# Kernel tuning notes

Measured on AMD Instinct MI355X. Metric: run time of the kernel, lower is better.

## Reference

```python
import jax, jax.numpy as jnp
import numpy as np

D_MODEL = 768
NUM_HEADS = 8
HEAD_DIM = D_MODEL // NUM_HEADS


def setup_inputs() -> dict:
    key = jax.random.key(0)
    ks = jax.random.split(key, 5)
    B, N = 4, 2048
    scale = 1.0 / np.sqrt(D_MODEL)
    return {
        "x": jax.random.normal(ks[0], (B, N, D_MODEL), dtype=jnp.float32),
        "W_qkv": jax.random.normal(ks[1], (D_MODEL, 3 * D_MODEL), dtype=jnp.float32) * scale,
        "b_qkv": jax.random.normal(ks[2], (3 * D_MODEL,), dtype=jnp.float32) * 0.01,
        "W_out": jax.random.normal(ks[3], (D_MODEL, D_MODEL), dtype=jnp.float32) * scale,
        "b_out": jax.random.normal(ks[4], (D_MODEL,), dtype=jnp.float32) * 0.01,
    }


def reference(x, W_qkv, b_qkv, W_out, b_out):
    B, N, _ = x.shape
    H, Dh = NUM_HEADS, HEAD_DIM
    # fused QKV projection: [B,N,3*D] -> [3,B,H,N,Dh]
    qkv = (x @ W_qkv + b_qkv).reshape(B, N, 3, H, Dh).transpose(2, 0, 3, 1, 4)
    q, k, v = qkv[0], qkv[1], qkv[2]
    # full NxN attention, as in the original (no masking)
    scores = jnp.einsum("bhnd,bhmd->bhnm", q, k) / jnp.sqrt(jnp.float32(Dh)).astype(x.dtype)
    weights = jax.nn.softmax(scores, axis=-1)
    out = jnp.einsum("bhnm,bhmd->bhnd", weights, v)  # [B,H,N,Dh]
    out = out.transpose(0, 2, 1, 3).reshape(B, N, H * Dh)
    return out @ W_out + b_out
```

## Files before the change

kernel.cpp:

```cpp
#include <hip/hip_runtime.h>
#include <hip/hip_bf16.h>
#include <math.h>

#define BB      4
#define NN      2048
#define DM      768
#define NH      8
#define DHH     96
#define BH      (BB*NH)
#define MROWS   (BB*NN)
#define NC_QKV  (3*DM)

typedef short v8s  __attribute__((ext_vector_type(8)));
typedef float v16f __attribute__((ext_vector_type(16)));
typedef unsigned int u32;

#define SCQ 0.14724599350930152f

static __device__ __forceinline__ ushort f2bf(float f) {
    __hip_bfloat16 h = __float2bfloat16(f);
    return *reinterpret_cast<ushort*>(&h);
}

static __device__ __forceinline__ void gload_lds16(const ushort* g, ushort* l) {
    __builtin_amdgcn_global_load_lds(
        (const __attribute__((address_space(1))) void*)g,
        (__attribute__((address_space(3))) void*)l, 16, 0, 0);
}

static __device__ __forceinline__ v8s pack_frag(u32 a, u32 b, u32 c, u32 d) {
    union { u32 u[4]; v8s s; } x;
    x.u[0] = a; x.u[1] = b; x.u[2] = c; x.u[3] = d;
    return x.s;
}

__global__ __launch_bounds__(256)
void conv_bf16(const float* __restrict__ in, ushort* __restrict__ out, int n8)
{
    int i = blockIdx.x * 256 + threadIdx.x;
    if (i >= n8) return;
    const float4* p = reinterpret_cast<const float4*>(in) + (size_t)i * 2;
    float4 a = p[0], b = p[1];
    ushort r[8] = {f2bf(a.x), f2bf(a.y), f2bf(a.z), f2bf(a.w),
                   f2bf(b.x), f2bf(b.y), f2bf(b.z), f2bf(b.w)};
    *reinterpret_cast<v8s*>(out + (size_t)i * 8) = *reinterpret_cast<v8s*>(r);
}

__global__ __launch_bounds__(256)
void convT_bf16(const float* __restrict__ W, ushort* __restrict__ Wt, int K, int N)
{
    __shared__ ushort t[32][33];
    const int k0 = blockIdx.x * 32, n0 = blockIdx.y * 32;
    const int tx = threadIdx.x & 31, ty = threadIdx.x >> 5;
    #pragma unroll
    for (int r = ty; r < 32; r += 8)
        t[tx][r] = f2bf(W[(size_t)(k0 + r) * N + n0 + tx]);
    __syncthreads();
    #pragma unroll
    for (int r = ty; r < 32; r += 8)
        Wt[(size_t)(n0 + r) * K + k0 + tx] = t[r][tx];
}

template<int SCATTER>
__global__ __launch_bounds__(256)
void gemm_mfma(const ushort* __restrict__ A, const ushort* __restrict__ Bt,
               const float* __restrict__ bias, void* __restrict__ outp,
               int K, int Ncols)
{
    __shared__ ushort As[8192];
    __shared__ ushort Bs[8192];

    const int tid  = threadIdx.x;
    const int lane = tid & 63;
    const int wv   = tid >> 6;
    const int l31  = lane & 31;
    const int lhi  = lane >> 5;
    const int wr   = wv >> 1, wc = wv & 1;
    const int row0 = blockIdx.x * 128;
    const int col0 = blockIdx.y * 128;

    v16f acc[2][2];
    #pragma unroll
    for (int mi = 0; mi < 2; ++mi)
        #pragma unroll
        for (int nj = 0; nj < 2; ++nj)
            #pragma unroll
            for (int i = 0; i < 16; ++i) acc[mi][nj][i] = 0.0f;

    for (int k0 = 0; k0 < K; k0 += 64) {
        #pragma unroll
        for (int c = 0; c < 4; ++c) {
            const int idx = (c * 4 + wv) * 64 + lane;
            const int s = idx >> 7, r = idx & 127;
            gload_lds16(&A [(size_t)(row0 + r) * K + k0 + s * 8], &As[(size_t)(c * 4 + wv) * 512]);
            gload_lds16(&Bt[(size_t)(col0 + r) * K + k0 + s * 8], &Bs[(size_t)(c * 4 + wv) * 512]);
        }
        __syncthreads();

        #pragma unroll
        for (int s16 = 0; s16 < 4; ++s16) {
            const int ks = s16 * 2 + lhi;
            v8s a0 = *reinterpret_cast<const v8s*>(&As[(size_t)(ks * 128 + 64 * wr + l31) * 8]);
            v8s a1 = *reinterpret_cast<const v8s*>(&As[(size_t)(ks * 128 + 64 * wr + 32 + l31) * 8]);
            v8s b0 = *reinterpret_cast<const v8s*>(&Bs[(size_t)(ks * 128 + 64 * wc + l31) * 8]);
            v8s b1 = *reinterpret_cast<const v8s*>(&Bs[(size_t)(ks * 128 + 64 * wc + 32 + l31) * 8]);
            acc[0][0] = __builtin_amdgcn_mfma_f32_32x32x16_bf16(a0, b0, acc[0][0], 0, 0, 0);
            acc[0][1] = __builtin_amdgcn_mfma_f32_32x32x16_bf16(a0, b1, acc[0][1], 0, 0, 0);
            acc[1][0] = __builtin_amdgcn_mfma_f32_32x32x16_bf16(a1, b0, acc[1][0], 0, 0, 0);
            acc[1][1] = __builtin_amdgcn_mfma_f32_32x32x16_bf16(a1, b1, acc[1][1], 0, 0, 0);
        }
        __syncthreads();
    }

    #pragma unroll
    for (int nj = 0; nj < 2; ++nj) {
        const int c = col0 + 64 * wc + 32 * nj + l31;
        const float bv = bias[c];
        #pragma unroll
        for (int mi = 0; mi < 2; ++mi) {
            #pragma unroll
            for (int r = 0; r < 16; ++r) {
                const int m = row0 + 64 * wr + 32 * mi + (r & 3) + 8 * (r >> 2) + 4 * lhi;
                float v = acc[mi][nj][r] + bv;
                if (SCATTER) {
                    const int s   = c / DM;
                    const int rem = c - s * DM;
                    const int h   = rem / DHH;
                    const int d   = rem - h * DHH;
                    const int b   = m >> 11;
                    const int n   = m & (NN - 1);
                    if (s == 0) v *= SCQ;
                    ((ushort*)outp)[((size_t)(s * BH + b * NH + h) * NN + n) * DHH + d] = f2bf(v);
                } else {
                    ((float*)outp)[(size_t)m * Ncols + c] = v;
                }
            }
        }
    }
}

__global__ __launch_bounds__(256)
void attn_mfma(const ushort* __restrict__ qkv, ushort* __restrict__ attnout)
{
    __shared__ ushort Ks[2][6144];
    __shared__ ushort Vt[2][96][72];

    const int tid  = threadIdx.x;
    const int lane = tid & 63;
    const int wv   = tid >> 6;
    const int l31  = lane & 31;
    const int lhi  = lane >> 5;
    const int q0   = blockIdx.x * 128;
    const int bh   = blockIdx.y;
    const int b    = bh >> 3, h = bh & 7;

    const ushort* Qg = qkv + (size_t)bh * NN * DHH;
    const ushort* Kg = qkv + ((size_t)BH + bh) * NN * DHH;
    const ushort* Vg = qkv + ((size_t)2 * BH + bh) * NN * DHH;

    const int qr = q0 + wv * 32 + l31;
    v8s qf[6];
    #pragma unroll
    for (int kt = 0; kt < 6; ++kt)
        qf[kt] = *reinterpret_cast<const v8s*>(&Qg[(size_t)qr * DHH + kt * 16 + lhi * 8]);

    v16f o[3];
    #pragma unroll
    for (int dt = 0; dt < 3; ++dt)
        #pragma unroll
        for (int i = 0; i < 16; ++i) o[dt][i] = 0.0f;
    float dsum = 0.0f;

    {
        v8s kr[3], vr[3];
        #pragma unroll
        for (int i = 0; i < 3; ++i) {
            kr[i] = *reinterpret_cast<const v8s*>(&Kg[(size_t)lane * DHH + (wv * 3 + i) * 8]);
            vr[i] = *reinterpret_cast<const v8s*>(&Vg[(size_t)lane * DHH + (i * 4 + wv) * 8]);
        }
        #pragma unroll
        for (int i = 0; i < 3; ++i) {
            *reinterpret_cast<v8s*>(&Ks[0][(wv * 3 + i) * 512 + lane * 8]) = kr[i];
            #pragma unroll
            for (int j = 0; j < 8; ++j)
                Vt[0][(i * 4 + wv) * 8 + j][lane] = (ushort)vr[i][j];
        }
    }
    __syncthreads();

    for (int t = 0; t < 32; ++t) {
        const int cur = t & 1, nxt = cur ^ 1;
        const int kbase = (t + 1) * 64;

        v8s kr0, kr1, kr2, vr0, vr1, vr2;
        if (t < 31) {
            const ushort* krow = &Kg[(size_t)(kbase + lane) * DHH];
            const ushort* vrow = &Vg[(size_t)(kbase + lane) * DHH];
            kr0 = *reinterpret_cast<const v8s*>(&krow[(wv * 3 + 0) * 8]);
            kr1 = *reinterpret_cast<const v8s*>(&krow[(wv * 3 + 1) * 8]);
            kr2 = *reinterpret_cast<const v8s*>(&krow[(wv * 3 + 2) * 8]);
            vr0 = *reinterpret_cast<const v8s*>(&vrow[(0 * 4 + wv) * 8]);
            vr1 = *reinterpret_cast<const v8s*>(&vrow[(1 * 4 + wv) * 8]);
            vr2 = *reinterpret_cast<const v8s*>(&vrow[(2 * 4 + wv) * 8]);
        }

        v8s pfrag[4];
        #pragma unroll
        for (int ct = 0; ct < 2; ++ct) {
            v16f s;
            #pragma unroll
            for (int i = 0; i < 16; ++i) s[i] = 0.0f;
            #pragma unroll
            for (int kt = 0; kt < 6; ++kt) {
                v8s kf = *reinterpret_cast<const v8s*>(
                    &Ks[cur][((kt * 2 + lhi) * 64 + ct * 32 + l31) * 8]);
                s = __builtin_amdgcn_mfma_f32_32x32x16_bf16(kf, qf[kt], s, 0, 0, 0);
            }
            float e[16];
            #pragma unroll
            for (int r = 0; r < 16; ++r) {
                e[r] = exp2f(s[r]);
                dsum += e[r];
            }
            u32 w[8];
            #pragma unroll
            for (int i = 0; i < 8; ++i)
                w[i] = (u32)f2bf(e[2 * i]) | ((u32)f2bf(e[2 * i + 1]) << 16);
            const u32 t0 = __shfl_xor(lhi ? w[0] : w[2], 32, 64);
            const u32 t1 = __shfl_xor(lhi ? w[1] : w[3], 32, 64);
            const u32 t2 = __shfl_xor(lhi ? w[4] : w[6], 32, 64);
            const u32 t3 = __shfl_xor(lhi ? w[5] : w[7], 32, 64);
            pfrag[2 * ct + 0] = lhi ? pack_frag(t0, t1, w[2], w[3])
                                    : pack_frag(w[0], w[1], t0, t1);
            pfrag[2 * ct + 1] = lhi ? pack_frag(t2, t3, w[6], w[7])
                                    : pack_frag(w[4], w[5], t2, t3);
        }

        #pragma unroll
        for (int dt = 0; dt < 3; ++dt) {
            #pragma unroll
            for (int ks = 0; ks < 4; ++ks) {
                v8s va = *reinterpret_cast<const v8s*>(
                    &Vt[cur][dt * 32 + l31][ks * 16 + lhi * 8]);
                o[dt] = __builtin_amdgcn_mfma_f32_32x32x16_bf16(va, pfrag[ks], o[dt], 0, 0, 0);
            }
        }

        if (t < 31) {
            *reinterpret_cast<v8s*>(&Ks[nxt][(wv * 3 + 0) * 512 + lane * 8]) = kr0;
            *reinterpret_cast<v8s*>(&Ks[nxt][(wv * 3 + 1) * 512 + lane * 8]) = kr1;
            *reinterpret_cast<v8s*>(&Ks[nxt][(wv * 3 + 2) * 512 + lane * 8]) = kr2;
            #pragma unroll
            for (int j = 0; j < 8; ++j) Vt[nxt][(0 * 4 + wv) * 8 + j][lane] = (ushort)vr0[j];
            #pragma unroll
            for (int j = 0; j < 8; ++j) Vt[nxt][(1 * 4 + wv) * 8 + j][lane] = (ushort)vr1[j];
            #pragma unroll
            for (int j = 0; j < 8; ++j) Vt[nxt][(2 * 4 + wv) * 8 + j][lane] = (ushort)vr2[j];
        }
        __syncthreads();
    }

    dsum += __shfl_xor(dsum, 32, 64);
    const float inv = 1.0f / dsum;

    const int n = q0 + wv * 32 + l31;
    ushort* orow = attnout + ((size_t)(b * NN + n)) * DM + h * DHH;
    #pragma unroll
    for (int dt = 0; dt < 3; ++dt) {
        #pragma unroll
        for (int g = 0; g < 4; ++g) {
            const int d0 = dt * 32 + 8 * g + 4 * lhi;
            u32 w0 = (u32)f2bf(o[dt][4 * g + 0] * inv) | ((u32)f2bf(o[dt][4 * g + 1] * inv) << 16);
            u32 w1 = (u32)f2bf(o[dt][4 * g + 2] * inv) | ((u32)f2bf(o[dt][4 * g + 3] * inv) << 16);
            uint2 pk; pk.x = w0; pk.y = w1;
            *reinterpret_cast<uint2*>(&orow[d0]) = pk;
        }
    }
}

extern "C" void kernel_launch(void* const* d_in, const int* in_sizes, int n_in,
                              void* d_out, int out_size, void* d_ws, size_t ws_size,
                              hipStream_t stream)
{
    (void)in_sizes; (void)n_in; (void)out_size; (void)ws_size;
    const float* x    = (const float*)d_in[0];
    const float* Wqkv = (const float*)d_in[1];
    const float* bqkv = (const float*)d_in[2];
    const float* Wout = (const float*)d_in[3];
    const float* bout = (const float*)d_in[4];
    float* out = (float*)d_out;

    ushort* qkv   = (ushort*)d_ws;
    ushort* ao    = qkv   + (size_t)3 * BH * NN * DHH;
    ushort* xbf   = ao    + (size_t)MROWS * DM;
    ushort* wqkvt = xbf   + (size_t)MROWS * DM;
    ushort* woutt = wqkvt + (size_t)DM * NC_QKV;

    dim3 blk(256);

    conv_bf16<<<dim3(MROWS * DM / 8 / 256), blk, 0, stream>>>(x, xbf, MROWS * DM / 8);
    convT_bf16<<<dim3(DM / 32, NC_QKV / 32), blk, 0, stream>>>(Wqkv, wqkvt, DM, NC_QKV);
    convT_bf16<<<dim3(DM / 32, DM / 32), blk, 0, stream>>>(Wout, woutt, DM, DM);

    gemm_mfma<1><<<dim3(MROWS / 128, NC_QKV / 128), blk, 0, stream>>>(
        xbf, wqkvt, bqkv, (void*)qkv, DM, NC_QKV);

    attn_mfma<<<dim3(NN / 128, BH), blk, 0, stream>>>(qkv, ao);

    gemm_mfma<0><<<dim3(MROWS / 128, DM / 128), blk, 0, stream>>>(
        ao, woutt, bout, (void*)out, DM, DM);
}
```

Baseline: 208.3 us.

## Double-buffer GEMM LDS tiles, remap blocks for XCD locality, add MFMA priority hints

The GEMM kernel now double-buffers its A/B LDS tiles, issuing the next k-tile's global-to-LDS loads before computing on the current one. This drops one barrier per iteration and overlaps loads with MFMA. Both GEMM and attention remap the linear block id so that blocks sharing operand rows or the same (batch, head) land on the same XCD (id & 7), aiming for better L2 reuse. The attention loop also raises wave priority around its MFMA sections. The costs are doubled LDS in the GEMM, which may reduce occupancy, and remap formulas that assume grid sizes divisible by 8.

```diff
diff --git a/kernel.cpp b/kernel.cpp
--- a/kernel.cpp
+++ b/kernel.cpp
@@ -67,8 +67,8 @@
                const float* __restrict__ bias, void* __restrict__ outp,
                int K, int Ncols)
 {
-    __shared__ ushort As[8192];
-    __shared__ ushort Bs[8192];
+    __shared__ ushort As[2][8192];
+    __shared__ ushort Bs[2][8192];
 
     const int tid  = threadIdx.x;
     const int lane = tid & 63;
@@ -76,8 +76,17 @@
     const int l31  = lane & 31;
     const int lhi  = lane >> 5;
     const int wr   = wv >> 1, wc = wv & 1;
-    const int row0 = blockIdx.x * 128;
-    const int col0 = blockIdx.y * 128;
+
+    const int ny   = gridDim.y;
+    const int id   = blockIdx.y * gridDim.x + blockIdx.x;
+    const int c8   = id & 7;
+    const int j    = id >> 3;
+    const int hy   = (j >= (ny >> 1) * 8) ? 1 : 0;
+    const int w    = j - hy * (ny >> 1) * 8;
+    const int bx   = c8 * 8 + (w & 7);
+    const int by   = hy * (ny >> 1) + (w >> 3);
+    const int row0 = bx * 128;
+    const int col0 = by * 128;
 
     v16f acc[2][2];
     #pragma unroll
@@ -87,23 +96,34 @@
             #pragma unroll
             for (int i = 0; i < 16; ++i) acc[mi][nj][i] = 0.0f;
 
-    for (int k0 = 0; k0 < K; k0 += 64) {
-        #pragma unroll
-        for (int c = 0; c < 4; ++c) {
-            const int idx = (c * 4 + wv) * 64 + lane;
-            const int s = idx >> 7, r = idx & 127;
-            gload_lds16(&A [(size_t)(row0 + r) * K + k0 + s * 8], &As[(size_t)(c * 4 + wv) * 512]);
-            gload_lds16(&Bt[(size_t)(col0 + r) * K + k0 + s * 8], &Bs[(size_t)(c * 4 + wv) * 512]);
-        }
-        __syncthreads();
+#define STAGE_G(bsel, kk) do {                                                  \
+    _Pragma("unroll")                                                           \
+    for (int c = 0; c < 4; ++c) {                                               \
+        const int g   = c * 4 + wv;                                             \
+        const int idx = g * 64 + lane;                                          \
+        const int ss  = idx >> 7, rr = idx & 127;                               \
+        gload_lds16(&A [(size_t)(row0 + rr) * K + (kk) + ss * 8],               \
+                    &As[bsel][g * 512]);                                        \
+        gload_lds16(&Bt[(size_t)(col0 + rr) * K + (kk) + ss * 8],               \
+                    &Bs[bsel][g * 512]);                                        \
+    }                                                                           \
+} while (0)
+
+    STAGE_G(0, 0);
+    __syncthreads();
+
+    const int nk = K >> 6;
+    for (int t = 0; t < nk; ++t) {
+        const int cur = t & 1;
+        if (t + 1 < nk) STAGE_G(cur ^ 1, (t + 1) << 6);
 
         #pragma unroll
         for (int s16 = 0; s16 < 4; ++s16) {
             const int ks = s16 * 2 + lhi;
-            v8s a0 = *reinterpret_cast<const v8s*>(&As[(size_t)(ks * 128 + 64 * wr + l31) * 8]);
-            v8s a1 = *reinterpret_cast<const v8s*>(&As[(size_t)(ks * 128 + 64 * wr + 32 + l31) * 8]);
-            v8s b0 = *reinterpret_cast<const v8s*>(&Bs[(size_t)(ks * 128 + 64 * wc + l31) * 8]);
-            v8s b1 = *reinterpret_cast<const v8s*>(&Bs[(size_t)(ks * 128 + 64 * wc + 32 + l31) * 8]);
+            v8s a0 = *reinterpret_cast<const v8s*>(&As[cur][(size_t)(ks * 128 + 64 * wr + l31) * 8]);
+            v8s a1 = *reinterpret_cast<const v8s*>(&As[cur][(size_t)(ks * 128 + 64 * wr + 32 + l31) * 8]);
+            v8s b0 = *reinterpret_cast<const v8s*>(&Bs[cur][(size_t)(ks * 128 + 64 * wc + l31) * 8]);
+            v8s b1 = *reinterpret_cast<const v8s*>(&Bs[cur][(size_t)(ks * 128 + 64 * wc + 32 + l31) * 8]);
             acc[0][0] = __builtin_amdgcn_mfma_f32_32x32x16_bf16(a0, b0, acc[0][0], 0, 0, 0);
             acc[0][1] = __builtin_amdgcn_mfma_f32_32x32x16_bf16(a0, b1, acc[0][1], 0, 0, 0);
             acc[1][0] = __builtin_amdgcn_mfma_f32_32x32x16_bf16(a1, b0, acc[1][0], 0, 0, 0);
@@ -111,6 +131,7 @@
         }
         __syncthreads();
     }
+#undef STAGE_G
 
     #pragma unroll
     for (int nj = 0; nj < 2; ++nj) {
@@ -150,8 +171,12 @@
     const int wv   = tid >> 6;
     const int l31  = lane & 31;
     const int lhi  = lane >> 5;
-    const int q0   = blockIdx.x * 128;
-    const int bh   = blockIdx.y;
+
+    const int id   = blockIdx.y * gridDim.x + blockIdx.x;
+    const int c8   = id & 7;
+    const int j    = id >> 3;
+    const int bh   = c8 * 4 + (j >> 4);
+    const int q0   = (j & 15) * 128;
     const int b    = bh >> 3, h = bh & 7;
 
     const ushort* Qg = qkv + (size_t)bh * NN * DHH;
@@ -182,8 +207,8 @@
         for (int i = 0; i < 3; ++i) {
             *reinterpret_cast<v8s*>(&Ks[0][(wv * 3 + i) * 512 + lane * 8]) = kr[i];
             #pragma unroll
-            for (int j = 0; j < 8; ++j)
-                Vt[0][(i * 4 + wv) * 8 + j][lane] = (ushort)vr[i][j];
+            for (int j2 = 0; j2 < 8; ++j2)
+                Vt[0][(i * 4 + wv) * 8 + j2][lane] = (ushort)vr[i][j2];
         }
     }
     __syncthreads();
@@ -210,12 +235,14 @@
             v16f s;
             #pragma unroll
             for (int i = 0; i < 16; ++i) s[i] = 0.0f;
+            __builtin_amdgcn_s_setprio(1);
             #pragma unroll
             for (int kt = 0; kt < 6; ++kt) {
                 v8s kf = *reinterpret_cast<const v8s*>(
                     &Ks[cur][((kt * 2 + lhi) * 64 + ct * 32 + l31) * 8]);
                 s = __builtin_amdgcn_mfma_f32_32x32x16_bf16(kf, qf[kt], s, 0, 0, 0);
             }
+            __builtin_amdgcn_s_setprio(0);
             float e[16];
             #pragma unroll
             for (int r = 0; r < 16; ++r) {
@@ -236,6 +263,7 @@
                                     : pack_frag(w[4], w[5], t2, t3);
         }
 
+        __builtin_amdgcn_s_setprio(1);
         #pragma unroll
         for (int dt = 0; dt < 3; ++dt) {
             #pragma unroll
@@ -245,17 +273,18 @@
                 o[dt] = __builtin_amdgcn_mfma_f32_32x32x16_bf16(va, pfrag[ks], o[dt], 0, 0, 0);
             }
         }
+        __builtin_amdgcn_s_setprio(0);
 
         if (t < 31) {
             *reinterpret_cast<v8s*>(&Ks[nxt][(wv * 3 + 0) * 512 + lane * 8]) = kr0;
             *reinterpret_cast<v8s*>(&Ks[nxt][(wv * 3 + 1) * 512 + lane * 8]) = kr1;
             *reinterpret_cast<v8s*>(&Ks[nxt][(wv * 3 + 2) * 512 + lane * 8]) = kr2;
             #pragma unroll
-            for (int j = 0; j < 8; ++j) Vt[nxt][(0 * 4 + wv) * 8 + j][lane] = (ushort)vr0[j];
-            #pragma unroll
-            for (int j = 0; j < 8; ++j) Vt[nxt][(1 * 4 + wv) * 8 + j][lane] = (ushort)vr1[j];
-            #pragma unroll
-            for (int j = 0; j < 8; ++j) Vt[nxt][(2 * 4 + wv) * 8 + j][lane] = (ushort)vr2[j];
+            for (int j2 = 0; j2 < 8; ++j2) Vt[nxt][(0 * 4 + wv) * 8 + j2][lane] = (ushort)vr0[j2];
+            #pragma unroll
+            for (int j2 = 0; j2 < 8; ++j2) Vt[nxt][(1 * 4 + wv) * 8 + j2][lane] = (ushort)vr1[j2];
+            #pragma unroll
+            for (int j2 = 0; j2 < 8; ++j2) Vt[nxt][(2 * 4 + wv) * 8 + j2][lane] = (ushort)vr2[j2];
         }
         __syncthreads();
     }
```

Measured after the change: 208.3 us. No clear change (-0.0%).
